# Performance work log

Measured on AMD Instinct MI355X. Metric: run time of the kernel, lower is better.

The kernel has to match this reference:

```python
import jax, jax.numpy as jnp
import numpy as np

B, P, C = 32, 8, 2048
D, H, W = 9, 11, 9
L = D * H * W  # 891
HID = C * P // 2  # 8192


def setup_inputs() -> dict:
    key = jax.random.key(0)
    k_x, k1w, k1b, k2w, k2b = jax.random.split(key, 5)
    x = jax.random.normal(k_x, (B, C, D, H, W), dtype=jnp.float32)
    fc1_w = jax.random.normal(k1w, (HID, C), dtype=jnp.float32) * 0.02
    fc1_b = jax.random.normal(k1b, (HID,), dtype=jnp.float32) * 0.02
    fc2_w = jax.random.normal(k2w, (C * P, HID), dtype=jnp.float32) * 0.02
    fc2_b = jax.random.normal(k2b, (C * P,), dtype=jnp.float32) * 0.02
    return {"x": x, "fc1_w": fc1_w, "fc1_b": fc1_b, "fc2_w": fc2_w, "fc2_b": fc2_b}


def reference(x, fc1_w, fc1_b, fc2_w, fc2_b):
    b = x.shape[0]
    # global average pool over the 9x11x9 volume -> (B, C)
    pooled = x.reshape(b, C, L).mean(axis=-1)
    h = jax.nn.sigmoid(pooled @ fc1_w.T + fc1_b)
    g = jax.nn.sigmoid(h @ fc2_w.T + fc2_b)          # (B, P*C)
    grouping_result = g.reshape(b, P, C)               # unfold(-1, C, C)
    # fused weighted channel reduction: avoids (B, P, C, 891) intermediate.
    # original: (grouping * conv_matrix) then AdaptiveAvgPool3d((891,1,1))
    # == mean over channels of grouping[b,p,c] * x[b,c,l]
    flat = x.reshape(b, C, L)
    weighted = jnp.einsum('bpc,bcl->bpl', grouping_result, flat) / C
    weighted = weighted.reshape(b, P, D, H, W)
    return (grouping_result, weighted)
```

## Files before the change

kernel.cpp:

```cpp
#include <hip/hip_runtime.h>
#include <hip/hip_bf16.h>

#define BB 32
#define CC 2048
#define LL 891
#define PP 8
#define HIDN 8192
#define NOUT 16384

typedef __attribute__((ext_vector_type(4))) float f32x4;
typedef __attribute__((ext_vector_type(8))) __bf16 bf16x8;

__global__ __launch_bounds__(256) void pool_kernel(const float* __restrict__ x,
                                                   __hip_bfloat16* __restrict__ pooled) {
  int wid = threadIdx.x >> 6, lane = threadIdx.x & 63;
  int row = blockIdx.x * 4 + wid;
  const float* r = x + (long)row * LL;
  float s = 0.f;
  for (int i = lane; i < LL; i += 64) s += r[i];
#pragma unroll
  for (int off = 32; off > 0; off >>= 1) s += __shfl_xor(s, off);
  if (lane == 0) pooled[row] = __float2bfloat16(s * (1.0f / (float)LL));
}

__device__ __forceinline__ unsigned int bfbits(float f) {
  unsigned int x = __builtin_bit_cast(unsigned int, f);
  return (x + 0x7fffu + ((x >> 16) & 1u)) >> 16;
}

__device__ __forceinline__ int swz(int row, int kb) {
  return row * 128 + (kb ^ ((row & 7) << 4));
}

__global__ __launch_bounds__(256) void fc_kernel(const __hip_bfloat16* __restrict__ A,
                                                 const float* __restrict__ W,
                                                 float* __restrict__ partial,
                                                 int N, int K, int kc) {
  __shared__ alignas(16) char Al[32 * 128];
  __shared__ alignas(16) char Bl[64 * 128];
  int tid = threadIdx.x;
  int n0 = blockIdx.x * 64;
  int k0 = blockIdx.y * kc;
  int ar = tid >> 3;
  int br = tid >> 2;
  int bk = (tid & 3) * 16;
  int lane = tid & 63, wv = tid >> 6;
  int r16 = lane & 15, kg = lane >> 4;

  const __hip_bfloat16* Ap = A + (long)ar * K + k0 + (tid & 7) * 8;
  const float* Wp = W + (long)(n0 + br) * K + k0 + bk;

  f32x4 acc0 = {0.f, 0.f, 0.f, 0.f};
  f32x4 acc1 = {0.f, 0.f, 0.f, 0.f};

  for (int ks = 0; ks < kc; ks += 64) {
    int4 av = *(const int4*)(Ap + ks);
    float4 f0 = *(const float4*)(Wp + ks);
    float4 f1 = *(const float4*)(Wp + ks + 4);
    float4 f2 = *(const float4*)(Wp + ks + 8);
    float4 f3 = *(const float4*)(Wp + ks + 12);
    int4 w0, w1;
    w0.x = (int)(bfbits(f0.x) | (bfbits(f0.y) << 16));
    w0.y = (int)(bfbits(f0.z) | (bfbits(f0.w) << 16));
    w0.z = (int)(bfbits(f1.x) | (bfbits(f1.y) << 16));
    w0.w = (int)(bfbits(f1.z) | (bfbits(f1.w) << 16));
    w1.x = (int)(bfbits(f2.x) | (bfbits(f2.y) << 16));
    w1.y = (int)(bfbits(f2.z) | (bfbits(f2.w) << 16));
    w1.z = (int)(bfbits(f3.x) | (bfbits(f3.y) << 16));
    w1.w = (int)(bfbits(f3.z) | (bfbits(f3.w) << 16));

    __syncthreads();
    *(int4*)(Al + swz(ar, (tid & 7) * 16)) = av;
    *(int4*)(Bl + swz(br, (tid & 3) * 32)) = w0;
    *(int4*)(Bl + swz(br, (tid & 3) * 32 + 16)) = w1;
    __syncthreads();

#pragma unroll
    for (int kh = 0; kh < 2; ++kh) {
      int kb = kh * 64 + kg * 16;
      bf16x8 a0 = __builtin_bit_cast(bf16x8, *(const int4*)(Al + swz(r16, kb)));
      bf16x8 a1 = __builtin_bit_cast(bf16x8, *(const int4*)(Al + swz(16 + r16, kb)));
      bf16x8 bv = __builtin_bit_cast(bf16x8, *(const int4*)(Bl + swz(wv * 16 + r16, kb)));
      acc0 = __builtin_amdgcn_mfma_f32_16x16x32_bf16(a0, bv, acc0, 0, 0, 0);
      acc1 = __builtin_amdgcn_mfma_f32_16x16x32_bf16(a1, bv, acc1, 0, 0, 0);
    }
  }

  long base = (long)blockIdx.y * 32 * N + n0 + wv * 16 + r16;
#pragma unroll
  for (int j = 0; j < 4; ++j) {
    int row = kg * 4 + j;
    partial[base + (long)row * N] = acc0[j];
    partial[base + (long)(row + 16) * N] = acc1[j];
  }
}

__global__ __launch_bounds__(256) void fc_reduce_kernel(const float* __restrict__ part,
                                                        int nsplit, int MN, int N,
                                                        const float* __restrict__ bias,
                                                        float* __restrict__ outF,
                                                        __hip_bfloat16* __restrict__ outB) {
  int idx = blockIdx.x * 256 + threadIdx.x;
  if (idx >= MN) return;
  float s = 0.f;
  for (int i = 0; i < nsplit; ++i) s += part[(long)i * MN + idx];
  s += bias[idx & (N - 1)];
  float v = 1.f / (1.f + __expf(-s));
  if (outF) outF[idx] = v;
  if (outB) outB[idx] = __float2bfloat16(v);
}

__global__ __launch_bounds__(256) void ein_partial_kernel(const float* __restrict__ x,
                                                          const float* __restrict__ g,
                                                          float* __restrict__ part) {
  int l = blockIdx.x * 256 + threadIdx.x;
  int b = blockIdx.y;
  int s = blockIdx.z;
  int c0 = s * 256;
  const float* xp = x + ((long)b * CC + c0) * LL + l;
  const float* gp = g + (long)b * NOUT + c0;
  bool act = l < LL;
  float acc[PP] = {0.f, 0.f, 0.f, 0.f, 0.f, 0.f, 0.f, 0.f};
  for (int i = 0; i < 256; ++i) {
    float xv = act ? xp[(long)i * LL] : 0.f;
#pragma unroll
    for (int p = 0; p < PP; ++p) acc[p] += gp[p * CC + i] * xv;
  }
  if (act) {
    float* pp = part + (long)(s * BB + b) * PP * LL + l;
#pragma unroll
    for (int p = 0; p < PP; ++p) pp[(long)p * LL] = acc[p];
  }
}

__global__ __launch_bounds__(256) void ein_reduce_kernel(const float* __restrict__ part,
                                                         float* __restrict__ outw) {
  int idx = blockIdx.x * 256 + threadIdx.x;
  float s = 0.f;
#pragma unroll
  for (int i = 0; i < 8; ++i) s += part[(long)i * (BB * PP * LL) + idx];
  outw[idx] = s * (1.0f / (float)CC);
}

extern "C" void kernel_launch(void* const* d_in, const int* in_sizes, int n_in,
                              void* d_out, int out_size, void* d_ws, size_t ws_size,
                              hipStream_t stream) {
  const float* x     = (const float*)d_in[0];
  const float* fc1_w = (const float*)d_in[1];
  const float* fc1_b = (const float*)d_in[2];
  const float* fc2_w = (const float*)d_in[3];
  const float* fc2_b = (const float*)d_in[4];
  float* out = (float*)d_out;

  char* ws = (char*)d_ws;
  __hip_bfloat16* pooled = (__hip_bfloat16*)ws;
  __hip_bfloat16* hbuf   = (__hip_bfloat16*)(ws + 131072);
  float* part            = (float*)(ws + 655360);

  pool_kernel<<<BB * CC / 4, 256, 0, stream>>>(x, pooled);

  fc_kernel<<<dim3(HIDN / 64, 4), 256, 0, stream>>>(pooled, fc1_w, part, HIDN, CC, CC / 4);
  fc_reduce_kernel<<<BB * HIDN / 256, 256, 0, stream>>>(part, 4, BB * HIDN, HIDN, fc1_b,
                                                        nullptr, hbuf);

  fc_kernel<<<dim3(NOUT / 64, 4), 256, 0, stream>>>(hbuf, fc2_w, part, NOUT, HIDN, HIDN / 4);
  fc_reduce_kernel<<<BB * NOUT / 256, 256, 0, stream>>>(part, 4, BB * NOUT, NOUT, fc2_b,
                                                        out, nullptr);

  ein_partial_kernel<<<dim3(4, BB, 8), 256, 0, stream>>>(x, out, part);
  ein_reduce_kernel<<<BB * PP * LL / 256, 256, 0, stream>>>(part, out + BB * PP * CC);
}
```

Baseline: 286.2 us.

## Drop LDS staging in FC GEMM, vectorize pooling, raise FC1 split-K

The FC kernel now has each wavefront load its weight and activation fragments straight from global memory into MFMA operands. This removes the shared-memory staging and both barriers per k-step, at the cost of more scattered global loads and the A operand being re-read by every wave. The pooling kernel switches to aligned float4 loads with scalar head and tail handling. FC1 split-K goes from 4 to 8 to add parallelism, and the einsum inner loop gets an unroll hint.

After: 285.4 us. No clear change (-0.3%).

```diff
diff --git a/kernel.cpp b/kernel.cpp
--- a/kernel.cpp
+++ b/kernel.cpp
@@ -16,8 +16,17 @@
   int wid = threadIdx.x >> 6, lane = threadIdx.x & 63;
   int row = blockIdx.x * 4 + wid;
   const float* r = x + (long)row * LL;
+  int align = (4 - ((row * 3) & 3)) & 3;
+  int nvec = (LL - align) >> 2;
+  int rem = LL - align - (nvec << 2);
+  const float4* v = (const float4*)(r + align);
   float s = 0.f;
-  for (int i = lane; i < LL; i += 64) s += r[i];
+  for (int i = lane; i < nvec; i += 64) {
+    float4 q = v[i];
+    s += (q.x + q.y) + (q.z + q.w);
+  }
+  if (lane < align) s += r[lane];
+  if (lane < rem) s += r[align + (nvec << 2) + lane];
 #pragma unroll
   for (int off = 32; off > 0; off >>= 1) s += __shfl_xor(s, off);
   if (lane == 0) pooled[row] = __float2bfloat16(s * (1.0f / (float)LL));
@@ -28,65 +37,39 @@
   return (x + 0x7fffu + ((x >> 16) & 1u)) >> 16;
 }
 
-__device__ __forceinline__ int swz(int row, int kb) {
-  return row * 128 + (kb ^ ((row & 7) << 4));
-}
-
 __global__ __launch_bounds__(256) void fc_kernel(const __hip_bfloat16* __restrict__ A,
                                                  const float* __restrict__ W,
                                                  float* __restrict__ partial,
                                                  int N, int K, int kc) {
-  __shared__ alignas(16) char Al[32 * 128];
-  __shared__ alignas(16) char Bl[64 * 128];
-  int tid = threadIdx.x;
-  int n0 = blockIdx.x * 64;
+  int lane = threadIdx.x & 63, wv = threadIdx.x >> 6;
+  int n0 = blockIdx.x * 64 + wv * 16;
   int k0 = blockIdx.y * kc;
-  int ar = tid >> 3;
-  int br = tid >> 2;
-  int bk = (tid & 3) * 16;
-  int lane = tid & 63, wv = tid >> 6;
-  int r16 = lane & 15, kg = lane >> 4;
+  int r = lane & 15, kg = lane >> 4;
 
-  const __hip_bfloat16* Ap = A + (long)ar * K + k0 + (tid & 7) * 8;
-  const float* Wp = W + (long)(n0 + br) * K + k0 + bk;
+  const float* Wp = W + (long)(n0 + r) * K + k0 + kg * 8;
+  const __hip_bfloat16* Ap0 = A + (long)r * K + k0 + kg * 8;
+  const __hip_bfloat16* Ap1 = Ap0 + 16 * (long)K;
 
   f32x4 acc0 = {0.f, 0.f, 0.f, 0.f};
   f32x4 acc1 = {0.f, 0.f, 0.f, 0.f};
 
-  for (int ks = 0; ks < kc; ks += 64) {
-    int4 av = *(const int4*)(Ap + ks);
-    float4 f0 = *(const float4*)(Wp + ks);
-    float4 f1 = *(const float4*)(Wp + ks + 4);
-    float4 f2 = *(const float4*)(Wp + ks + 8);
-    float4 f3 = *(const float4*)(Wp + ks + 12);
-    int4 w0, w1;
-    w0.x = (int)(bfbits(f0.x) | (bfbits(f0.y) << 16));
-    w0.y = (int)(bfbits(f0.z) | (bfbits(f0.w) << 16));
-    w0.z = (int)(bfbits(f1.x) | (bfbits(f1.y) << 16));
-    w0.w = (int)(bfbits(f1.z) | (bfbits(f1.w) << 16));
-    w1.x = (int)(bfbits(f2.x) | (bfbits(f2.y) << 16));
-    w1.y = (int)(bfbits(f2.z) | (bfbits(f2.w) << 16));
-    w1.z = (int)(bfbits(f3.x) | (bfbits(f3.y) << 16));
-    w1.w = (int)(bfbits(f3.z) | (bfbits(f3.w) << 16));
-
-    __syncthreads();
-    *(int4*)(Al + swz(ar, (tid & 7) * 16)) = av;
-    *(int4*)(Bl + swz(br, (tid & 3) * 32)) = w0;
-    *(int4*)(Bl + swz(br, (tid & 3) * 32 + 16)) = w1;
-    __syncthreads();
-
-#pragma unroll
-    for (int kh = 0; kh < 2; ++kh) {
-      int kb = kh * 64 + kg * 16;
-      bf16x8 a0 = __builtin_bit_cast(bf16x8, *(const int4*)(Al + swz(r16, kb)));
-      bf16x8 a1 = __builtin_bit_cast(bf16x8, *(const int4*)(Al + swz(16 + r16, kb)));
-      bf16x8 bv = __builtin_bit_cast(bf16x8, *(const int4*)(Bl + swz(wv * 16 + r16, kb)));
-      acc0 = __builtin_amdgcn_mfma_f32_16x16x32_bf16(a0, bv, acc0, 0, 0, 0);
-      acc1 = __builtin_amdgcn_mfma_f32_16x16x32_bf16(a1, bv, acc1, 0, 0, 0);
-    }
+#pragma unroll 2
+  for (int ks = 0; ks < kc; ks += 32) {
+    float4 w0 = *(const float4*)(Wp + ks);
+    float4 w1 = *(const float4*)(Wp + ks + 4);
+    int4 a0 = *(const int4*)(Ap0 + ks);
+    int4 a1 = *(const int4*)(Ap1 + ks);
+    int4 bw;
+    bw.x = (int)(bfbits(w0.x) | (bfbits(w0.y) << 16));
+    bw.y = (int)(bfbits(w0.z) | (bfbits(w0.w) << 16));
+    bw.z = (int)(bfbits(w1.x) | (bfbits(w1.y) << 16));
+    bw.w = (int)(bfbits(w1.z) | (bfbits(w1.w) << 16));
+    bf16x8 bv = __builtin_bit_cast(bf16x8, bw);
+    acc0 = __builtin_amdgcn_mfma_f32_16x16x32_bf16(__builtin_bit_cast(bf16x8, a0), bv, acc0, 0, 0, 0);
+    acc1 = __builtin_amdgcn_mfma_f32_16x16x32_bf16(__builtin_bit_cast(bf16x8, a1), bv, acc1, 0, 0, 0);
   }
 
-  long base = (long)blockIdx.y * 32 * N + n0 + wv * 16 + r16;
+  long base = (long)blockIdx.y * 32 * N + n0 + r;
 #pragma unroll
   for (int j = 0; j < 4; ++j) {
     int row = kg * 4 + j;
@@ -121,6 +104,7 @@
   const float* gp = g + (long)b * NOUT + c0;
   bool act = l < LL;
   float acc[PP] = {0.f, 0.f, 0.f, 0.f, 0.f, 0.f, 0.f, 0.f};
+#pragma unroll 4
   for (int i = 0; i < 256; ++i) {
     float xv = act ? xp[(long)i * LL] : 0.f;
 #pragma unroll
@@ -159,8 +143,8 @@
 
   pool_kernel<<<BB * CC / 4, 256, 0, stream>>>(x, pooled);
 
-  fc_kernel<<<dim3(HIDN / 64, 4), 256, 0, stream>>>(pooled, fc1_w, part, HIDN, CC, CC / 4);
-  fc_reduce_kernel<<<BB * HIDN / 256, 256, 0, stream>>>(part, 4, BB * HIDN, HIDN, fc1_b,
+  fc_kernel<<<dim3(HIDN / 64, 8), 256, 0, stream>>>(pooled, fc1_w, part, HIDN, CC, CC / 8);
+  fc_reduce_kernel<<<BB * HIDN / 256, 256, 0, stream>>>(part, 8, BB * HIDN, HIDN, fc1_b,
                                                         nullptr, hbuf);
 
   fc_kernel<<<dim3(NOUT / 64, 4), 256, 0, stream>>>(hbuf, fc2_w, part, NOUT, HIDN, HIDN / 4);
```
